# Optimization experiments

Measured on AMD Instinct MI355X. Metric: run time of the kernel, lower is better.

## Reference

```python
import jax, jax.numpy as jnp
import numpy as np

N = 400000   # nodes; must equal E because the original code computes `out + x` with out per-edge
E = 400000   # edges
HID = 128
HEADS = 4
NEG_SLOPE = 0.01  # torch F.leaky_relu default


def setup_inputs() -> dict:
    key = jax.random.key(0)
    k1, k2, k3, k4 = jax.random.split(key, 4)
    x = jax.random.normal(k1, (N, HID), dtype=jnp.float32)
    edge_index = jax.random.randint(k2, (2, E), 0, N, dtype=jnp.int64)
    # xavier-uniform-ish scale for the attention parameter [1, heads, 2*hidden]
    lim_a = float(np.sqrt(6.0 / (1 + HEADS * 2 * HID)))
    attention = jax.random.uniform(k3, (1, HEADS, 2 * HID), jnp.float32, -lim_a, lim_a)
    lim_w = float(np.sqrt(1.0 / (HID * HEADS)))
    W = jax.random.uniform(k4, (HID, HID * HEADS), jnp.float32, -lim_w, lim_w)
    b = jnp.zeros((HID,), jnp.float32)
    return {"x": x, "edge_index": edge_index, "attention": attention, "W": W, "b": b}


def _scatter_softmax(s, seg, num_segments):
    # softmax over edges grouped by destination node index `seg` (axis 0)
    m = jax.lax.stop_gradient(jax.ops.segment_max(s, seg, num_segments=num_segments))
    ex = jnp.exp(s - m[seg])
    denom = jax.ops.segment_sum(ex, seg, num_segments=num_segments)
    return ex / denom[seg]


def reference(x, edge_index, attention, W, b):
    row, col = edge_index[0], edge_index[1]
    # [E, 2*HID] per-edge concatenated features
    ef = jnp.concatenate([x[row], x[col]], axis=-1)
    # per-head scores: (ef[:,None,:] * attention).sum(-1) -> [E, HEADS]
    scores = jnp.einsum('ef,hf->eh', ef, attention[0])
    scores = jax.nn.leaky_relu(scores, NEG_SLOPE)
    scores = jax.nn.softmax(scores, axis=1)      # softmax across heads (as in source)
    # dropout(p=0.1) -> identity in eval mode
    alpha = _scatter_softmax(scores, row, N)     # [E, HEADS] per-destination softmax
    # per-head weighted source features, concatenated over heads -> [E, HEADS*HID]
    feats = (alpha[:, :, None] * x[col][:, None, :]).reshape(E, HEADS * HID)
    out = feats @ W.T + b                        # Linear(hidden*heads -> hidden)
    return out + x
```

## Files before the change

### kernel.cpp

```cpp
#include <hip/hip_runtime.h>

#define NN 400000
#define NE 400000

typedef __attribute__((ext_vector_type(4))) float f32x4;
typedef __attribute__((ext_vector_type(8))) short s16x8;
typedef unsigned short ushort_t;

__device__ __forceinline__ ushort_t f2bf(float f) {
    union { float f; unsigned int u; } c;
    c.f = f;
    unsigned int u = c.u;
    u = u + 0x7fffu + ((u >> 16) & 1u);
    return (ushort_t)(u >> 16);
}
__device__ __forceinline__ float bf2f(ushort_t v) {
    union { unsigned int u; float f; } c;
    c.u = ((unsigned int)v) << 16;
    return c.f;
}

__global__ void k_prep(const float* __restrict__ W, ushort_t* __restrict__ wbf,
                       const float* __restrict__ att, ushort_t* __restrict__ attB,
                       const int* __restrict__ ei_raw, int* __restrict__ flag,
                       float* __restrict__ denom) {
    if (blockIdx.x < 256) {
        const int i = blockIdx.x * 256 + threadIdx.x;
        wbf[i] = f2bf(W[i]);
    } else if (blockIdx.x == 256) {
        const int t = threadIdx.x;
        const int ks = t >> 6, lane = t & 63;
        const int col = lane & 15, kg = lane >> 4;
        const int jb = ks * 32 + kg * 8;
        s16x8 pk;
#pragma unroll
        for (int m = 0; m < 8; m++) {
            float v = 0.f;
            if (col < 4)      v = att[col * 256 + jb + m];
            else if (col < 8) v = att[(col - 4) * 256 + 128 + jb + m];
            pk[m] = (short)f2bf(v);
        }
        *(s16x8*)(attB + (size_t)(ks * 64 + lane) * 8) = pk;
    } else if (blockIdx.x == 257) {
        if (threadIdx.x < 64) {
            const int v = ei_raw[2 * threadIdx.x + 1];
            const unsigned long long b = __ballot(v != 0);
            if (threadIdx.x == 0) flag[0] = (b == 0ULL) ? 1 : 0;
        }
    } else {
        const int i = (blockIdx.x - 258) * 256 + threadIdx.x;
        if (i < NN) *(f32x4*)(denom + (size_t)i * 4) = (f32x4){0.f, 0.f, 0.f, 0.f};
    }
}

__global__ __launch_bounds__(256) void k_uv_mfma(
    const float* __restrict__ x, const ushort_t* __restrict__ attB,
    ushort_t* __restrict__ xbf, float* __restrict__ uv) {
    const int lane = threadIdx.x & 63;
    const int wv = threadIdx.x >> 6;
    const int kg = lane >> 4;

    s16x8 bfr[4];
#pragma unroll
    for (int ks = 0; ks < 4; ks++)
        bfr[ks] = *(const s16x8*)(attB + (size_t)(ks * 64 + lane) * 8);

    const f32x4 zero = {0.f, 0.f, 0.f, 0.f};
    const int ntiles = NN / 64;

#pragma unroll 1
    for (int tile = blockIdx.x; tile < ntiles; tile += gridDim.x) {
        const int n = tile * 64 + wv * 16 + (lane & 15);
        const float* xr = x + (size_t)n * 128 + kg * 8;
        ushort_t* xw = xbf + (size_t)n * 128 + kg * 8;

        s16x8 afr[4];
#pragma unroll
        for (int ks = 0; ks < 4; ks++) {
            const f32x4 a0 = __builtin_nontemporal_load((const f32x4*)(xr + ks * 32));
            const f32x4 a1 = __builtin_nontemporal_load((const f32x4*)(xr + ks * 32 + 4));
            s16x8 pk;
#pragma unroll
            for (int m = 0; m < 4; m++) { pk[m] = (short)f2bf(a0[m]); pk[4 + m] = (short)f2bf(a1[m]); }
            afr[ks] = pk;
            *(s16x8*)(xw + ks * 32) = pk;
        }
        f32x4 c = zero;
#pragma unroll
        for (int ks = 0; ks < 4; ks++)
            c = __builtin_amdgcn_mfma_f32_16x16x32_bf16(afr[ks], bfr[ks], c, 0, 0, 0);

        const int colc = lane & 15;
        if (colc < 8) {
#pragma unroll
            for (int r = 0; r < 4; r++) {
                const int nn = tile * 64 + wv * 16 + kg * 4 + r;
                uv[(size_t)nn * 8 + colc] = c[r];
            }
        }
    }
}

__global__ void k_edge(const int* __restrict__ ei_raw, const int* __restrict__ flag,
                       const float* __restrict__ uv, float* __restrict__ p,
                       float* __restrict__ denom, int* __restrict__ ei32) {
    const int e = blockIdx.x * 256 + threadIdx.x;
    if (e >= NE) return;
    const int f = flag[0];
    const int row = f ? ei_raw[2 * e] : ei_raw[e];
    const int col = f ? ei_raw[2 * (NE + e)] : ei_raw[NE + e];
    ei32[e] = row;
    ei32[NE + e] = col;
    const f32x4 u = *(const f32x4*)(uv + (size_t)row * 8);
    const f32x4 v = *(const f32x4*)(uv + (size_t)col * 8 + 4);
    float s[4];
    float mx = -1e30f;
#pragma unroll
    for (int h = 0; h < 4; h++) {
        float t = u[h] + v[h];
        t = t > 0.f ? t : 0.01f * t;
        s[h] = t;
        mx = fmaxf(mx, t);
    }
    float ex[4], sum = 0.f;
#pragma unroll
    for (int h = 0; h < 4; h++) { ex[h] = __expf(s[h] - mx); sum += ex[h]; }
    const float inv = 1.f / sum;
    f32x4 pv;
#pragma unroll
    for (int h = 0; h < 4; h++) pv[h] = __expf(ex[h] * inv);
    *(f32x4*)(p + (size_t)e * 4) = pv;
#pragma unroll
    for (int h = 0; h < 4; h++) atomicAdd(denom + (size_t)row * 4 + h, pv[h]);
}

__global__ void k_alpha(const int* __restrict__ ei, const float* __restrict__ p,
                        const float* __restrict__ denom, float* __restrict__ alpha4) {
    const int e = blockIdx.x * 256 + threadIdx.x;
    if (e >= NE) return;
    const int row = ei[e];
    const f32x4 pv = *(const f32x4*)(p + (size_t)e * 4);
    const f32x4 dv = *(const f32x4*)(denom + (size_t)row * 4);
    *(f32x4*)(alpha4 + (size_t)e * 4) = pv / dv;
}

__global__ __launch_bounds__(1024, 4) void k_gemm(
    const ushort_t* __restrict__ xbf, const int* __restrict__ ei,
    const float* __restrict__ alpha4, const ushort_t* __restrict__ wbf,
    const float* __restrict__ bias, float* __restrict__ out)
{
    __shared__ __align__(16) ushort_t Bsm[128 * 512];
    __shared__ __align__(16) ushort_t Asm[2][64 * 128];

    const int tid = threadIdx.x;
    const int lane = tid & 63;
    const int w = tid >> 6;
    const int eg = w & 1;
    const int cg = w >> 1;

    {
        const int icol = tid & 127, seg = tid >> 7;
        const ushort_t* src = wbf + icol * 512 + seg * 64;
#pragma unroll
        for (int m = 0; m < 8; m++) {
            const s16x8 v = *(const s16x8*)(src + m * 8);
            const int byte = icol * 1024 + ((seg * 128 + m * 16) ^ ((icol & 15) << 4));
            *(s16x8*)((char*)Bsm + byte) = v;
        }
    }
    const int icol = cg * 16 + (lane & 15);
    const float bias_r = bias[icol];

    const f32x4 zero = {0.f, 0.f, 0.f, 0.f};
    const int ntiles = NE / 64;
    const int stride = gridDim.x;

    auto STAGE = [&](int tt, int b) {
        const int rr = w * 4 + (lane >> 4);
        const int col = ei[NE + tt * 64 + rr];
        const int c = (lane & 15) ^ (rr & 15);
        const ushort_t* src = xbf + (size_t)col * 128 + c * 8;
        __builtin_amdgcn_global_load_lds(
            (const __attribute__((address_space(1))) unsigned int*)src,
            (__attribute__((address_space(3))) unsigned int*)((char*)Asm[b] + w * 1024),
            16, 0, 0);
    };

    int t = blockIdx.x;
    int cur = 0;
    if (t < ntiles) STAGE(t, 0);

#pragma unroll 1
    for (; t < ntiles; t += stride) {
        __syncthreads();
        const int tn = t + stride;
        if (tn < ntiles) STAGE(tn, cur ^ 1);

        const f32x4 alp = *(const f32x4*)(alpha4 + (size_t)(t * 64 + eg * 32 + (lane & 31)) * 4);

        s16x8 af[2][4];
#pragma unroll
        for (int eb = 0; eb < 2; eb++) {
            const int rr = eg * 32 + eb * 16 + (lane & 15);
#pragma unroll
            for (int ks = 0; ks < 4; ks++) {
                const int byte = rr * 256 + ((ks * 64 + (lane >> 4) * 16) ^ ((rr & 15) << 4));
                af[eb][ks] = *(const s16x8*)((const char*)Asm[cur] + byte);
            }
        }

        f32x4 fin[2];
        fin[0] = zero; fin[1] = zero;

#pragma unroll
        for (int h = 0; h < 4; h++) {
            s16x8 bfr[4];
#pragma unroll
            for (int ks = 0; ks < 4; ks++) {
                const int byte = icol * 1024 +
                    ((h * 256 + ks * 64 + (lane >> 4) * 16) ^ ((icol & 15) << 4));
                bfr[ks] = *(const s16x8*)((const char*)Bsm + byte);
            }
#pragma unroll
            for (int eb = 0; eb < 2; eb++) {
                f32x4 a = __builtin_amdgcn_mfma_f32_16x16x32_bf16(af[eb][0], bfr[0], zero, 0, 0, 0);
#pragma unroll
                for (int ks = 1; ks < 4; ks++)
                    a = __builtin_amdgcn_mfma_f32_16x16x32_bf16(af[eb][ks], bfr[ks], a, 0, 0, 0);
                f32x4 av;
#pragma unroll
                for (int r = 0; r < 4; r++)
                    av[r] = __shfl(alp[h], eb * 16 + (lane >> 4) * 4 + r, 64);
                fin[eb] += av * a;
            }
        }
#pragma unroll
        for (int eb = 0; eb < 2; eb++) {
#pragma unroll
            for (int r = 0; r < 4; r++) {
                const int e = t * 64 + eg * 32 + eb * 16 + (lane >> 4) * 4 + r;
                const size_t off = (size_t)e * 128 + icol;
                __builtin_nontemporal_store(fin[eb][r] + bias_r + bf2f(xbf[off]), &out[off]);
            }
        }
        cur ^= 1;
    }
}

extern "C" void kernel_launch(void* const* d_in, const int* in_sizes, int n_in,
                              void* d_out, int out_size, void* d_ws, size_t ws_size,
                              hipStream_t stream) {
    const float* x      = (const float*)d_in[0];
    const int*   ei_raw = (const int*)d_in[1];
    const float* att    = (const float*)d_in[2];
    const float* W      = (const float*)d_in[3];
    const float* b      = (const float*)d_in[4];
    float* out = (float*)d_out;

    char* ws = (char*)d_ws;
    float*    uv      = (float*)(ws);
    float*    p       = (float*)(ws + 12800000);
    float*    denom   = (float*)(ws + 19200000);
    float*    alpha4  = (float*)(ws + 25600000);
    ushort_t* wbf     = (ushort_t*)(ws + 32000000);
    int*      flag    = (int*)(ws + 32200000);
    ushort_t* attB    = (ushort_t*)(ws + 32200064);
    int*      ei32    = (int*)(ws + 32210048);
    ushort_t* xbf     = (ushort_t*)(ws + 35420224);

    k_prep<<<258 + (NN + 255) / 256, 256, 0, stream>>>(W, wbf, att, attB, ei_raw, flag, denom);
    k_uv_mfma<<<2048, 256, 0, stream>>>(x, attB, xbf, uv);
    k_edge<<<(NE + 255) / 256, 256, 0, stream>>>(ei_raw, flag, uv, p, denom, ei32);
    k_alpha<<<(NE + 255) / 256, 256, 0, stream>>>(ei32, p, denom, alpha4);
    k_gemm<<<256, 1024, 0, stream>>>(xbf, ei32, alpha4, wbf, b, out);
}
```

Before: 265.8 us.

## Keep W fragments in registers and give each wave all 64 edges

The gather-GEMM kernel changes from 1024-thread blocks, where wave pairs split the 64 edges, to 512-thread blocks. Each wave now owns 16 output columns across all 64 edges of a tile. The bf16 W fragments for all four heads are loaded from LDS into registers once, before the tile loop, instead of being re-read every tile. The barrier moves to the end of each iteration and the A-tile staging issues two async loads per wave. This removes repeated LDS traffic for B, but it halves the waves per CU and raises register pressure, which may reduce latency hiding for the memory-bound gather and store.

```diff
diff --git a/kernel.cpp b/kernel.cpp
--- a/kernel.cpp
+++ b/kernel.cpp
@@ -144,7 +144,7 @@
     *(f32x4*)(alpha4 + (size_t)e * 4) = pv / dv;
 }
 
-__global__ __launch_bounds__(1024, 4) void k_gemm(
+__global__ __launch_bounds__(512, 2) void k_gemm(
     const ushort_t* __restrict__ xbf, const int* __restrict__ ei,
     const float* __restrict__ alpha4, const ushort_t* __restrict__ wbf,
     const float* __restrict__ bias, float* __restrict__ out)
@@ -155,20 +155,19 @@
     const int tid = threadIdx.x;
     const int lane = tid & 63;
     const int w = tid >> 6;
-    const int eg = w & 1;
-    const int cg = w >> 1;
+    const int kg = lane >> 4;
 
     {
-        const int icol = tid & 127, seg = tid >> 7;
-        const ushort_t* src = wbf + icol * 512 + seg * 64;
-#pragma unroll
-        for (int m = 0; m < 8; m++) {
+        const int icol = tid >> 2, q = tid & 3;
+        const ushort_t* src = wbf + icol * 512 + q * 128;
+#pragma unroll
+        for (int m = 0; m < 16; m++) {
             const s16x8 v = *(const s16x8*)(src + m * 8);
-            const int byte = icol * 1024 + ((seg * 128 + m * 16) ^ ((icol & 15) << 4));
+            const int byte = icol * 1024 + ((q * 256 + m * 16) ^ ((icol & 15) << 4));
             *(s16x8*)((char*)Bsm + byte) = v;
         }
     }
-    const int icol = cg * 16 + (lane & 15);
+    const int icol = w * 16 + (lane & 15);
     const float bias_r = bias[icol];
 
     const f32x4 zero = {0.f, 0.f, 0.f, 0.f};
@@ -176,73 +175,71 @@
     const int stride = gridDim.x;
 
     auto STAGE = [&](int tt, int b) {
-        const int rr = w * 4 + (lane >> 4);
-        const int col = ei[NE + tt * 64 + rr];
-        const int c = (lane & 15) ^ (rr & 15);
-        const ushort_t* src = xbf + (size_t)col * 128 + c * 8;
-        __builtin_amdgcn_global_load_lds(
-            (const __attribute__((address_space(1))) unsigned int*)src,
-            (__attribute__((address_space(3))) unsigned int*)((char*)Asm[b] + w * 1024),
-            16, 0, 0);
+#pragma unroll
+        for (int i = 0; i < 2; i++) {
+            const int rr = w * 8 + i * 4 + (lane >> 4);
+            const int col = ei[NE + tt * 64 + rr];
+            const int c = (lane & 15) ^ (rr & 15);
+            const ushort_t* src = xbf + (size_t)col * 128 + c * 8;
+            __builtin_amdgcn_global_load_lds(
+                (const __attribute__((address_space(1))) unsigned int*)src,
+                (__attribute__((address_space(3))) unsigned int*)((char*)Asm[b] + w * 2048 + i * 1024),
+                16, 0, 0);
+        }
     };
 
     int t = blockIdx.x;
     int cur = 0;
     if (t < ntiles) STAGE(t, 0);
+    __syncthreads();
+
+    s16x8 bfr[4][4];
+#pragma unroll
+    for (int h = 0; h < 4; h++)
+#pragma unroll
+        for (int ks = 0; ks < 4; ks++) {
+            const int byte = icol * 1024 +
+                ((h * 256 + ks * 64 + kg * 16) ^ ((icol & 15) << 4));
+            bfr[h][ks] = *(const s16x8*)((const char*)Bsm + byte);
+        }
 
 #pragma unroll 1
     for (; t < ntiles; t += stride) {
-        __syncthreads();
         const int tn = t + stride;
         if (tn < ntiles) STAGE(tn, cur ^ 1);
 
-        const f32x4 alp = *(const f32x4*)(alpha4 + (size_t)(t * 64 + eg * 32 + (lane & 31)) * 4);
-
-        s16x8 af[2][4];
-#pragma unroll
-        for (int eb = 0; eb < 2; eb++) {
-            const int rr = eg * 32 + eb * 16 + (lane & 15);
+        const f32x4 alp = *(const f32x4*)(alpha4 + (size_t)(t * 64 + lane) * 4);
+
+#pragma unroll
+        for (int eb = 0; eb < 4; eb++) {
+            s16x8 af[4];
+            const int rr = eb * 16 + (lane & 15);
 #pragma unroll
             for (int ks = 0; ks < 4; ks++) {
-                const int byte = rr * 256 + ((ks * 64 + (lane >> 4) * 16) ^ ((rr & 15) << 4));
-                af[eb][ks] = *(const s16x8*)((const char*)Asm[cur] + byte);
-            }
-        }
-
-        f32x4 fin[2];
-        fin[0] = zero; fin[1] = zero;
-
-#pragma unroll
-        for (int h = 0; h < 4; h++) {
-            s16x8 bfr[4];
-#pragma unroll
-            for (int ks = 0; ks < 4; ks++) {
-                const int byte = icol * 1024 +
-                    ((h * 256 + ks * 64 + (lane >> 4) * 16) ^ ((icol & 15) << 4));
-                bfr[ks] = *(const s16x8*)((const char*)Bsm + byte);
-            }
-#pragma unroll
-            for (int eb = 0; eb < 2; eb++) {
-                f32x4 a = __builtin_amdgcn_mfma_f32_16x16x32_bf16(af[eb][0], bfr[0], zero, 0, 0, 0);
+                const int byte = rr * 256 + ((ks * 64 + kg * 16) ^ ((rr & 15) << 4));
+                af[ks] = *(const s16x8*)((const char*)Asm[cur] + byte);
+            }
+            f32x4 fin = zero;
+#pragma unroll
+            for (int h = 0; h < 4; h++) {
+                f32x4 a = __builtin_amdgcn_mfma_f32_16x16x32_bf16(af[0], bfr[h][0], zero, 0, 0, 0);
 #pragma unroll
                 for (int ks = 1; ks < 4; ks++)
-                    a = __builtin_amdgcn_mfma_f32_16x16x32_bf16(af[eb][ks], bfr[ks], a, 0, 0, 0);
+                    a = __builtin_amdgcn_mfma_f32_16x16x32_bf16(af[ks], bfr[h][ks], a, 0, 0, 0);
                 f32x4 av;
 #pragma unroll
                 for (int r = 0; r < 4; r++)
-                    av[r] = __shfl(alp[h], eb * 16 + (lane >> 4) * 4 + r, 64);
-                fin[eb] += av * a;
-            }
-        }
-#pragma unroll
-        for (int eb = 0; eb < 2; eb++) {
+                    av[r] = __shfl(alp[h], eb * 16 + kg * 4 + r, 64);
+                fin += av * a;
+            }
 #pragma unroll
             for (int r = 0; r < 4; r++) {
-                const int e = t * 64 + eg * 32 + eb * 16 + (lane >> 4) * 4 + r;
+                const int e = t * 64 + eb * 16 + kg * 4 + r;
                 const size_t off = (size_t)e * 128 + icol;
-                __builtin_nontemporal_store(fin[eb][r] + bias_r + bf2f(xbf[off]), &out[off]);
-            }
-        }
+                __builtin_nontemporal_store(fin[r] + bias_r + bf2f(xbf[off]), &out[off]);
+            }
+        }
+        __syncthreads();
         cur ^= 1;
     }
 }
@@ -272,5 +269,5 @@
     k_uv_mfma<<<2048, 256, 0, stream>>>(x, attB, xbf, uv);
     k_edge<<<(NE + 255) / 256, 256, 0, stream>>>(ei_raw, flag, uv, p, denom, ei32);
     k_alpha<<<(NE + 255) / 256, 256, 0, stream>>>(ei32, p, denom, alpha4);
-    k_gemm<<<256, 1024, 0, stream>>>(xbf, ei32, alpha4, wbf, b, out);
-}
+    k_gemm<<<256, 512, 0, stream>>>(xbf, ei32, alpha4, wbf, b, out);
+}
```

New measurement: 257.4 us. 1.03x faster.
